# Performance work log

Measured on AMD Instinct MI355X. Metric: run time of the kernel, lower is better.

Reference implementation:

```python
import jax, jax.numpy as jnp
import numpy as np

TEMPERATURE = 0.1
GAMMA = 0.5
LOSS_WEIGHT = 1.0
LINE_CLASS = 2
COS_EPS = 1e-8      # torch F.cosine_similarity eps
RADIUS = 1.0        # positive-pair spatial radius
SELF_EPS = 1e-6     # excludes self pairs (dist ~ 0) from positives
NCE_EPS = 1e-6


def _pairwise_dist(coords):
    # Euclidean cdist [N, N] with a sqrt that is safe at 0 (self pairs)
    sq = jnp.sum(coords * coords, axis=1)
    d2 = jnp.maximum(sq[:, None] + sq[None, :] - 2.0 * (coords @ coords.T), 0.0)
    safe = jnp.where(d2 > 0.0, d2, 1.0)
    return jnp.where(d2 > 0.0, jnp.sqrt(safe), 0.0)


def setup_inputs() -> dict:
    key = jax.random.key(0)
    k1, k2, k3 = jax.random.split(key, 3)
    N, D = 4096, 64
    features = jax.random.normal(k1, (N, D), dtype=jnp.float32)
    # uniform in a 10x10x10 box -> ~30 neighbors within radius 1.0 per point
    coords = jax.random.uniform(k2, (N, 3), dtype=jnp.float32) * 10.0
    labels = jax.random.randint(k3, (N,), 0, 3)  # class 2 == power line
    return {"features": features, "labels": labels, "coords": coords}


def reference(features, labels, coords):
    # Static-shape equivalent of boolean-indexing the line-class points:
    # weight w_i = 1 iff labels[i] == LINE_CLASS. All sums / means below are
    # restricted to line points via w, matching torch masked gather exactly.
    w = (labels == LINE_CLASS).astype(features.dtype)        # [N]
    M = jnp.sum(w)                                           # number of line points
    pair_w = w[:, None] * w[None, :]                         # [N, N]

    # cosine similarity matrix  [N, N]
    norms = jnp.maximum(jnp.linalg.norm(features, axis=1, keepdims=True), COS_EPS)
    fn = features / norms
    feat_sim = fn @ fn.T

    # spatial distance matrix and pos / neg pair masks  [N, N]
    coord_dist = _pairwise_dist(coords)
    pos_raw = ((coord_dist < RADIUS) & (coord_dist > SELF_EPS)).astype(features.dtype)
    pos_w = pair_w * pos_raw
    neg_w = pair_w * (1.0 - pos_raw)   # ~pos_mask within line subset (incl. self)

    # InfoNCE over line points
    exp_sim = jnp.exp(feat_sim / TEMPERATURE)
    pos_sum = jnp.sum(exp_sim * pos_w, axis=1)               # [N]
    neg_sum = jnp.sum(exp_sim * neg_w, axis=1)               # [N]
    ratio = pos_sum / (neg_sum + pos_sum + NCE_EPS)
    per_point = -jnp.log(jnp.where(w > 0, ratio, 1.0))       # 0 for non-line pts
    info_nce = jnp.sum(per_point) / M                        # mean over line pts

    # continuity: mean over the M x M line-pair block
    feat_dist = 1.0 - feat_sim
    continuity = jnp.sum(jnp.abs(feat_dist - coord_dist) * pos_w) / (M * M)

    return (info_nce + GAMMA * continuity) * LOSS_WEIGHT
```

## Files before the change

kernel.cpp:

```cpp
#include <hip/hip_runtime.h>
#include <hip/hip_bf16.h>

#define LINE_CLASS 2
#define NJ 32

__global__ __launch_bounds__(1024) void compact_kernel(const int* __restrict__ labels,
                                                       const float* __restrict__ coords,
                                                       int N, int* __restrict__ idx,
                                                       int* __restrict__ Mout,
                                                       float4* __restrict__ cC) {
    __shared__ int wcnt[16];
    __shared__ int base;
    const int tid = threadIdx.x;
    const int wid = tid >> 6, lane = tid & 63;
    if (tid == 0) base = 0;
    __syncthreads();
    for (int s = 0; s < N; s += 1024) {
        const int i = s + tid;
        const bool p = (i < N) && (labels[i] == LINE_CLASS);
        const unsigned long long m = __ballot(p);
        if (lane == 0) wcnt[wid] = __popcll(m);
        __syncthreads();
        int off = base;
        for (int w = 0; w < wid; ++w) off += wcnt[w];
        off += __popcll(m & ((1ull << lane) - 1ull));
        if (p) idx[off] = i;
        __syncthreads();
        if (tid == 0) {
            int t = 0;
            for (int w = 0; w < 16; ++w) t += wcnt[w];
            base += t;
        }
        __syncthreads();
    }
    const int M = base;
    for (int b = tid; b < M; b += 1024) {
        const int i = idx[b];
        const float x = coords[i * 3 + 0];
        const float y = coords[i * 3 + 1];
        const float z = coords[i * 3 + 2];
        const float sq = fmaf(x, x, fmaf(y, y, z * z));
        cC[b] = make_float4(x, y, z, sq);
    }
    if (tid == 0) *Mout = M;
}

__global__ __launch_bounds__(256) void prep_kernel(const float* __restrict__ feat,
                                                   const int* __restrict__ idx,
                                                   const int* __restrict__ Mp,
                                                   float* __restrict__ fnC) {
    const int b = blockIdx.x * 4 + (threadIdx.x >> 6);
    const int d = threadIdx.x & 63;
    const int M = *Mp;
    if (b >= M) return;
    const int i = idx[b];
    const float v = feat[i * 64 + d];
    float ss = v * v;
    #pragma unroll
    for (int off = 32; off > 0; off >>= 1) ss += __shfl_xor(ss, off);
    const float dn = fmaxf(sqrtf(ss), 1e-8f);
    fnC[b * 64 + d] = v / dn;
}

__global__ __launch_bounds__(256) void pair_kernel(const float* __restrict__ fnC,
                                                   const float4* __restrict__ cC,
                                                   const int* __restrict__ Mp,
                                                   int N,
                                                   float* __restrict__ posp,
                                                   float* __restrict__ negp,
                                                   float* __restrict__ contp) {
    const int b  = blockIdx.x;
    const int js = blockIdx.y;
    const int tid = threadIdx.x;
    const int r = tid & 63;
    const int q = tid >> 6;
    const int M = *Mp;
    const int k = b * 64 + r;

    if (b * 64 >= M) {
        if (tid == 0) contp[b * NJ + js] = 0.0f;
        return;
    }
    const bool valid = (k < M);

    float4 f4[16];
    if (valid) {
        const float4* fr = (const float4*)(fnC + (size_t)k * 64);
        #pragma unroll
        for (int t = 0; t < 16; ++t) f4[t] = fr[t];
    } else {
        #pragma unroll
        for (int t = 0; t < 16; ++t) f4[t] = make_float4(0.f, 0.f, 0.f, 0.f);
    }
    const float4 ci = valid ? cC[k] : make_float4(0.f, 0.f, 0.f, 0.f);

    const int chunk = (M + NJ - 1) / NJ;
    const int j0 = js * chunk;
    const int j1 = (j0 + chunk < M) ? (j0 + chunk) : M;

    float pos = 0.0f, neg = 0.0f, cont = 0.0f;

    for (int j = j0 + q; j < j1; j += 4) {
        const int ju = __builtin_amdgcn_readfirstlane(j);
        const float4* __restrict__ fjv = (const float4*)(fnC + (size_t)ju * 64);
        float dot = 0.0f;
        #pragma unroll
        for (int t = 0; t < 16; ++t) {
            const float4 bv = fjv[t];
            dot = fmaf(f4[t].x, bv.x, dot);
            dot = fmaf(f4[t].y, bv.y, dot);
            dot = fmaf(f4[t].z, bv.z, dot);
            dot = fmaf(f4[t].w, bv.w, dot);
        }
        const float4 cj = cC[ju];
        const float cdot = fmaf(ci.x, cj.x, fmaf(ci.y, cj.y, ci.z * cj.z));
        float d2 = fmaxf(ci.w + cj.w - 2.0f * cdot, 0.0f);
        const float dist = (d2 > 0.0f) ? sqrtf(d2) : 0.0f;
        const float e = expf(dot * 10.0f);
        const bool isPos = (dist < 1.0f) && (dist > 1e-6f);
        if (isPos) {
            pos += e;
            if (valid) cont += fabsf((1.0f - dot) - dist);
        } else {
            neg += e;
        }
    }

    __shared__ float sp[4][64];
    __shared__ float sn[4][64];
    __shared__ float sc[256];
    sp[q][r] = pos;
    sn[q][r] = neg;
    sc[tid] = cont;
    __syncthreads();
    if (q == 0) {
        const float P  = sp[0][r] + sp[1][r] + sp[2][r] + sp[3][r];
        const float Ng = sn[0][r] + sn[1][r] + sn[2][r] + sn[3][r];
        posp[(size_t)js * N + k] = P;
        negp[(size_t)js * N + k] = Ng;
    }
    for (int s = 128; s > 0; s >>= 1) {
        if (tid < s) sc[tid] += sc[tid + s];
        __syncthreads();
    }
    if (tid == 0) contp[b * NJ + js] = sc[0];
}

__global__ __launch_bounds__(1024) void final_kernel(const float* __restrict__ posp,
                                                     const float* __restrict__ negp,
                                                     const float* __restrict__ contp,
                                                     const int* __restrict__ Mp,
                                                     int N, int NB,
                                                     float* __restrict__ out) {
    const int tid = threadIdx.x;
    const int M = *Mp;
    float nce = 0.0f;
    for (int k = tid; k < M; k += 1024) {
        float P = 0.0f, Ng = 0.0f;
        for (int js = 0; js < NJ; ++js) {
            P  += posp[(size_t)js * N + k];
            Ng += negp[(size_t)js * N + k];
        }
        const float ratio = fmaxf(P / (Ng + P + 1e-6f), 1e-38f);
        nce += -logf(ratio);
    }
    float cont = 0.0f;
    const int nslots = NB * NJ;
    for (int c = tid; c < nslots; c += 1024) cont += contp[c];

    __shared__ float r1[1024];
    __shared__ float r2[1024];
    r1[tid] = nce;
    r2[tid] = cont;
    __syncthreads();
    for (int s = 512; s > 0; s >>= 1) {
        if (tid < s) { r1[tid] += r1[tid + s]; r2[tid] += r2[tid + s]; }
        __syncthreads();
    }
    if (tid == 0) {
        const float Mf = (float)M;
        out[0] = (r1[0] / Mf + 0.5f * (r2[0] / (Mf * Mf))) * 1.0f;
    }
}

extern "C" void kernel_launch(void* const* d_in, const int* in_sizes, int n_in,
                              void* d_out, int out_size, void* d_ws, size_t ws_size,
                              hipStream_t stream) {
    const float* feat   = (const float*)d_in[0];
    const int*   labels = (const int*)  d_in[1];
    const float* coords = (const float*)d_in[2];
    const int N = in_sizes[1];

    char* ws = (char*)d_ws;
    int*    Mp      = (int*)   (ws + 0);
    int*    idx     = (int*)   (ws + 1024);
    float4* cC      = (float4*)(ws + 32768);
    float*  fnC     = (float*) (ws + 131072);
    float*  posp    = (float*) (ws + 2097152);
    float*  negp    = (float*) (ws + 2621440);
    float*  contp   = (float*) (ws + 3145728);

    const int NB = (N + 63) / 64;

    compact_kernel<<<1, 1024, 0, stream>>>(labels, coords, N, idx, Mp, cC);
    prep_kernel<<<(N + 3) / 4, 256, 0, stream>>>(feat, idx, Mp, fnC);
    pair_kernel<<<dim3(NB, NJ), 256, 0, stream>>>(fnC, cC, Mp, N, posp, negp, contp);
    final_kernel<<<1, 1024, 0, stream>>>(posp, negp, contp, Mp, N, NB, (float*)d_out);
}
```

Measured before the change: 93.53 us.

## Fuse compaction and normalization into pair kernel with LDS-staged column tiles

Removes the separate single-block compaction and feature-normalization kernels. Every pair block now recomputes the label prefix scan itself, gathers and normalizes its own row features and its column chunk directly from the inputs, and stages the column features and coordinates in shared memory. This cuts two kernel launches and the serial single-block compaction, at the cost of redundant label scans in every block and heavier shared-memory use (about 34KB per block). Chunks are capped at MAXCHUNK, which assumes M <= 4096.

```diff
diff --git a/kernel.cpp b/kernel.cpp
--- a/kernel.cpp
+++ b/kernel.cpp
@@ -3,141 +3,162 @@
 
 #define LINE_CLASS 2
 #define NJ 32
-
-__global__ __launch_bounds__(1024) void compact_kernel(const int* __restrict__ labels,
-                                                       const float* __restrict__ coords,
-                                                       int N, int* __restrict__ idx,
-                                                       int* __restrict__ Mout,
-                                                       float4* __restrict__ cC) {
-    __shared__ int wcnt[16];
-    __shared__ int base;
+#define MAXCHUNK 128
+
+__global__ __launch_bounds__(256) void pair_kernel(const float* __restrict__ feat,
+                                                   const int* __restrict__ labels,
+                                                   const float* __restrict__ coords,
+                                                   int N,
+                                                   int* __restrict__ Mout,
+                                                   float* __restrict__ posp,
+                                                   float* __restrict__ negp,
+                                                   float* __restrict__ contp) {
+    const int b   = blockIdx.x;
+    const int js  = blockIdx.y;
     const int tid = threadIdx.x;
-    const int wid = tid >> 6, lane = tid & 63;
-    if (tid == 0) base = 0;
-    __syncthreads();
-    for (int s = 0; s < N; s += 1024) {
-        const int i = s + tid;
-        const bool p = (i < N) && (labels[i] == LINE_CLASS);
-        const unsigned long long m = __ballot(p);
-        if (lane == 0) wcnt[wid] = __popcll(m);
-        __syncthreads();
-        int off = base;
-        for (int w = 0; w < wid; ++w) off += wcnt[w];
-        off += __popcll(m & ((1ull << lane) - 1ull));
-        if (p) idx[off] = i;
-        __syncthreads();
-        if (tid == 0) {
-            int t = 0;
-            for (int w = 0; w < 16; ++w) t += wcnt[w];
-            base += t;
-        }
-        __syncthreads();
-    }
-    const int M = base;
-    for (int b = tid; b < M; b += 1024) {
-        const int i = idx[b];
+    const int r   = tid & 63;
+    const int q   = tid >> 6;
+
+    __shared__ int    scnt[256];
+    __shared__ int    ownIdx[64];
+    __shared__ int    jIdx[MAXCHUNK];
+    __shared__ float4 jcC[MAXCHUNK];
+    __shared__ float  fj[MAXCHUNK * 64];
+    __shared__ float  sp[4][64], sn[4][64], sc[256];
+
+    const int EPT = (N + 255) / 256;
+    const int i0  = tid * EPT;
+    unsigned long long bits = 0ull;
+    for (int u = 0; u < EPT; ++u) {
+        const int i = i0 + u;
+        if (i < N && labels[i] == LINE_CLASS) bits |= (1ull << u);
+    }
+    const int cnt = __popcll(bits);
+    scnt[tid] = cnt;
+    __syncthreads();
+    for (int s = 1; s < 256; s <<= 1) {
+        int v = scnt[tid];
+        if (tid >= s) v += scnt[tid - s];
+        __syncthreads();
+        scnt[tid] = v;
+        __syncthreads();
+    }
+    const int M = scnt[255];
+    if (b == 0 && js == 0 && tid == 0) *Mout = M;
+
+    const int own0 = b * 64;
+    if (own0 >= M) return;
+
+    int chunk = (M + NJ - 1) / NJ;
+    if (chunk > MAXCHUNK) chunk = MAXCHUNK;
+    const int j0   = js * chunk;
+    const int j1   = (j0 + chunk < M) ? (j0 + chunk) : M;
+    const int jcnt = j1 - j0;
+    const int k    = own0 + r;
+
+    if (jcnt <= 0) {
+        if (q == 0) {
+            posp[(size_t)js * N + k] = 0.0f;
+            negp[(size_t)js * N + k] = 0.0f;
+        }
+        if (tid == 0) contp[b * NJ + js] = 0.0f;
+        return;
+    }
+
+    int pos = scnt[tid] - cnt;
+    for (int u = 0; u < EPT; ++u) {
+        if (bits & (1ull << u)) {
+            const int i  = i0 + u;
+            const int dO = pos - own0;
+            if (dO >= 0 && dO < 64) ownIdx[dO] = i;
+            const int dJ = pos - j0;
+            if (dJ >= 0 && dJ < jcnt) jIdx[dJ] = i;
+            ++pos;
+        }
+    }
+    __syncthreads();
+
+    for (int t = tid; t < jcnt; t += 256) {
+        const int i = jIdx[t];
         const float x = coords[i * 3 + 0];
         const float y = coords[i * 3 + 1];
         const float z = coords[i * 3 + 2];
-        const float sq = fmaf(x, x, fmaf(y, y, z * z));
-        cC[b] = make_float4(x, y, z, sq);
-    }
-    if (tid == 0) *Mout = M;
-}
-
-__global__ __launch_bounds__(256) void prep_kernel(const float* __restrict__ feat,
-                                                   const int* __restrict__ idx,
-                                                   const int* __restrict__ Mp,
-                                                   float* __restrict__ fnC) {
-    const int b = blockIdx.x * 4 + (threadIdx.x >> 6);
-    const int d = threadIdx.x & 63;
-    const int M = *Mp;
-    if (b >= M) return;
-    const int i = idx[b];
-    const float v = feat[i * 64 + d];
-    float ss = v * v;
-    #pragma unroll
-    for (int off = 32; off > 0; off >>= 1) ss += __shfl_xor(ss, off);
-    const float dn = fmaxf(sqrtf(ss), 1e-8f);
-    fnC[b * 64 + d] = v / dn;
-}
-
-__global__ __launch_bounds__(256) void pair_kernel(const float* __restrict__ fnC,
-                                                   const float4* __restrict__ cC,
-                                                   const int* __restrict__ Mp,
-                                                   int N,
-                                                   float* __restrict__ posp,
-                                                   float* __restrict__ negp,
-                                                   float* __restrict__ contp) {
-    const int b  = blockIdx.x;
-    const int js = blockIdx.y;
-    const int tid = threadIdx.x;
-    const int r = tid & 63;
-    const int q = tid >> 6;
-    const int M = *Mp;
-    const int k = b * 64 + r;
-
-    if (b * 64 >= M) {
-        if (tid == 0) contp[b * NJ + js] = 0.0f;
-        return;
-    }
+        jcC[t] = make_float4(x, y, z, fmaf(x, x, fmaf(y, y, z * z)));
+    }
+    for (int jj = q; jj < jcnt; jj += 4) {
+        const int i = jIdx[jj];
+        const float v = feat[(size_t)i * 64 + r];
+        float ss = v * v;
+        #pragma unroll
+        for (int off = 32; off > 0; off >>= 1) ss += __shfl_xor(ss, off);
+        const float inv = 1.0f / fmaxf(sqrtf(ss), 1e-8f);
+        fj[jj * 64 + r] = v * inv;
+    }
+
     const bool valid = (k < M);
-
     float4 f4[16];
+    float4 ci;
     if (valid) {
-        const float4* fr = (const float4*)(fnC + (size_t)k * 64);
-        #pragma unroll
-        for (int t = 0; t < 16; ++t) f4[t] = fr[t];
+        const int i = ownIdx[r];
+        const float4* fr = (const float4*)(feat + (size_t)i * 64);
+        float ss = 0.0f;
+        #pragma unroll
+        for (int t = 0; t < 16; ++t) {
+            f4[t] = fr[t];
+            ss = fmaf(f4[t].x, f4[t].x, ss);
+            ss = fmaf(f4[t].y, f4[t].y, ss);
+            ss = fmaf(f4[t].z, f4[t].z, ss);
+            ss = fmaf(f4[t].w, f4[t].w, ss);
+        }
+        const float inv = 1.0f / fmaxf(sqrtf(ss), 1e-8f);
+        #pragma unroll
+        for (int t = 0; t < 16; ++t) {
+            f4[t].x *= inv; f4[t].y *= inv; f4[t].z *= inv; f4[t].w *= inv;
+        }
+        const float x = coords[i * 3 + 0];
+        const float y = coords[i * 3 + 1];
+        const float z = coords[i * 3 + 2];
+        ci = make_float4(x, y, z, fmaf(x, x, fmaf(y, y, z * z)));
     } else {
         #pragma unroll
         for (int t = 0; t < 16; ++t) f4[t] = make_float4(0.f, 0.f, 0.f, 0.f);
-    }
-    const float4 ci = valid ? cC[k] : make_float4(0.f, 0.f, 0.f, 0.f);
-
-    const int chunk = (M + NJ - 1) / NJ;
-    const int j0 = js * chunk;
-    const int j1 = (j0 + chunk < M) ? (j0 + chunk) : M;
-
-    float pos = 0.0f, neg = 0.0f, cont = 0.0f;
-
-    for (int j = j0 + q; j < j1; j += 4) {
-        const int ju = __builtin_amdgcn_readfirstlane(j);
-        const float4* __restrict__ fjv = (const float4*)(fnC + (size_t)ju * 64);
+        ci = make_float4(0.f, 0.f, 0.f, 0.f);
+    }
+    __syncthreads();
+
+    float pos_s = 0.0f, neg_s = 0.0f, cont_s = 0.0f;
+    for (int jj = q; jj < jcnt; jj += 4) {
+        const float4* __restrict__ fv = (const float4*)(fj + jj * 64);
         float dot = 0.0f;
         #pragma unroll
         for (int t = 0; t < 16; ++t) {
-            const float4 bv = fjv[t];
+            const float4 bv = fv[t];
             dot = fmaf(f4[t].x, bv.x, dot);
             dot = fmaf(f4[t].y, bv.y, dot);
             dot = fmaf(f4[t].z, bv.z, dot);
             dot = fmaf(f4[t].w, bv.w, dot);
         }
-        const float4 cj = cC[ju];
+        const float4 cj = jcC[jj];
         const float cdot = fmaf(ci.x, cj.x, fmaf(ci.y, cj.y, ci.z * cj.z));
-        float d2 = fmaxf(ci.w + cj.w - 2.0f * cdot, 0.0f);
+        const float d2 = fmaxf(ci.w + cj.w - 2.0f * cdot, 0.0f);
         const float dist = (d2 > 0.0f) ? sqrtf(d2) : 0.0f;
         const float e = expf(dot * 10.0f);
         const bool isPos = (dist < 1.0f) && (dist > 1e-6f);
         if (isPos) {
-            pos += e;
-            if (valid) cont += fabsf((1.0f - dot) - dist);
+            pos_s += e;
+            if (valid) cont_s += fabsf((1.0f - dot) - dist);
         } else {
-            neg += e;
-        }
-    }
-
-    __shared__ float sp[4][64];
-    __shared__ float sn[4][64];
-    __shared__ float sc[256];
-    sp[q][r] = pos;
-    sn[q][r] = neg;
-    sc[tid] = cont;
+            neg_s += e;
+        }
+    }
+
+    sp[q][r] = pos_s;
+    sn[q][r] = neg_s;
+    sc[tid]  = cont_s;
     __syncthreads();
     if (q == 0) {
-        const float P  = sp[0][r] + sp[1][r] + sp[2][r] + sp[3][r];
-        const float Ng = sn[0][r] + sn[1][r] + sn[2][r] + sn[3][r];
-        posp[(size_t)js * N + k] = P;
-        negp[(size_t)js * N + k] = Ng;
+        posp[(size_t)js * N + k] = sp[0][r] + sp[1][r] + sp[2][r] + sp[3][r];
+        negp[(size_t)js * N + k] = sn[0][r] + sn[1][r] + sn[2][r] + sn[3][r];
     }
     for (int s = 128; s > 0; s >>= 1) {
         if (tid < s) sc[tid] += sc[tid + s];
@@ -150,13 +171,14 @@
                                                      const float* __restrict__ negp,
                                                      const float* __restrict__ contp,
                                                      const int* __restrict__ Mp,
-                                                     int N, int NB,
+                                                     int N,
                                                      float* __restrict__ out) {
     const int tid = threadIdx.x;
     const int M = *Mp;
     float nce = 0.0f;
     for (int k = tid; k < M; k += 1024) {
         float P = 0.0f, Ng = 0.0f;
+        #pragma unroll
         for (int js = 0; js < NJ; ++js) {
             P  += posp[(size_t)js * N + k];
             Ng += negp[(size_t)js * N + k];
@@ -165,7 +187,8 @@
         nce += -logf(ratio);
     }
     float cont = 0.0f;
-    const int nslots = NB * NJ;
+    const int nact = (M + 63) / 64;
+    const int nslots = nact * NJ;
     for (int c = tid; c < nslots; c += 1024) cont += contp[c];
 
     __shared__ float r1[1024];
@@ -192,18 +215,14 @@
     const int N = in_sizes[1];
 
     char* ws = (char*)d_ws;
-    int*    Mp      = (int*)   (ws + 0);
-    int*    idx     = (int*)   (ws + 1024);
-    float4* cC      = (float4*)(ws + 32768);
-    float*  fnC     = (float*) (ws + 131072);
-    float*  posp    = (float*) (ws + 2097152);
-    float*  negp    = (float*) (ws + 2621440);
-    float*  contp   = (float*) (ws + 3145728);
+    int*   Mp    = (int*)  (ws + 0);
+    float* posp  = (float*)(ws + 1024);
+    float* negp  = (float*)(ws + 1024 + (size_t)4 * NJ * N);
+    float* contp = (float*)(ws + 1024 + (size_t)8 * NJ * N);
 
     const int NB = (N + 63) / 64;
 
-    compact_kernel<<<1, 1024, 0, stream>>>(labels, coords, N, idx, Mp, cC);
-    prep_kernel<<<(N + 3) / 4, 256, 0, stream>>>(feat, idx, Mp, fnC);
-    pair_kernel<<<dim3(NB, NJ), 256, 0, stream>>>(fnC, cC, Mp, N, posp, negp, contp);
-    final_kernel<<<1, 1024, 0, stream>>>(posp, negp, contp, Mp, N, NB, (float*)d_out);
+    pair_kernel<<<dim3(NB, NJ), 256, 0, stream>>>(feat, labels, coords, N,
+                                                  Mp, posp, negp, contp);
+    final_kernel<<<1, 1024, 0, stream>>>(posp, negp, contp, Mp, N, (float*)d_out);
 }
```

Result: slower. 108.1 us (+15.6%).
